# Optimization experiments

Measured on AMD Instinct MI355X. Metric: run time of the kernel, lower is better.

Reference implementation:

```python
import jax, jax.numpy as jnp
import numpy as np

B, N, DIM, HEADS = 8, 512, 512, 16
MAX_DIST, NG = 128, 32
RBF_STOP = 20.0
EPS = 1e-5


def _ln(x, g, b):
    m = jnp.mean(x, axis=-1, keepdims=True)
    v = jnp.mean((x - m) ** 2, axis=-1, keepdims=True)
    return (x - m) * jax.lax.rsqrt(v + EPS) * g + b


def setup_inputs() -> dict:
    key = jax.random.key(0)
    ks = jax.random.split(key, 12)
    d = DIM
    s = 0.02
    return {
        "x": jax.random.normal(ks[0], (B * N, d), jnp.float32),
        "dist_matrix": jax.random.randint(ks[1], (B, N, N), 0, MAX_DIST, jnp.int32),
        "dist_3d": jax.random.uniform(ks[2], (B, N, N), jnp.float32) * RBF_STOP,
        "norm1_g": jnp.ones((d,), jnp.float32),
        "norm1_b": jnp.zeros((d,), jnp.float32),
        "in_proj_w": jax.random.normal(ks[3], (3 * d, d), jnp.float32) * s,
        "in_proj_b": jnp.zeros((3 * d,), jnp.float32),
        "out_proj_w": jax.random.normal(ks[4], (d, d), jnp.float32) * s,
        "out_proj_b": jnp.zeros((d,), jnp.float32),
        "dist_emb": jax.random.normal(ks[5], (MAX_DIST, HEADS), jnp.float32) * s,
        "rbf_w": jax.random.normal(ks[6], (HEADS, NG), jnp.float32) * s,
        "rbf_b": jnp.zeros((HEADS,), jnp.float32),
        "norm2_g": jnp.ones((d,), jnp.float32),
        "norm2_b": jnp.zeros((d,), jnp.float32),
        "ffn_w1": jax.random.normal(ks[7], (4 * d, d), jnp.float32) * s,
        "ffn_b1": jnp.zeros((4 * d,), jnp.float32),
        "ffn_w2": jax.random.normal(ks[8], (d, 4 * d), jnp.float32) * s,
        "ffn_b2": jnp.zeros((d,), jnp.float32),
        "batch": jnp.repeat(jnp.arange(B, dtype=jnp.int32), N),
    }


def reference(x, dist_matrix, dist_3d, norm1_g, norm1_b, in_proj_w, in_proj_b,
              out_proj_w, out_proj_b, dist_emb, rbf_w, rbf_b, norm2_g, norm2_b,
              ffn_w1, ffn_b1, ffn_w2, ffn_b2, batch):
    b, n = dist_matrix.shape[0], dist_matrix.shape[1]
    d = x.shape[-1]
    dh = d // HEADS
    # equal-size graphs -> to_dense_batch is a reshape, mask all-true
    xd = x.reshape(b, n, d)

    # additive attention bias: shortest-path-distance embedding + RBF projection
    dc = jnp.clip(dist_matrix, 0, MAX_DIST - 1)
    bias_spd = dist_emb[dc]                                  # [b, n, n, H]
    offset = jnp.linspace(0.0, RBF_STOP, NG, dtype=jnp.float32)
    coeff = -0.5 / (RBF_STOP / (NG - 1)) ** 2
    rbf = jnp.exp(coeff * (dist_3d[..., None] - offset) ** 2)  # [b, n, n, NG]
    bias_3d = rbf @ rbf_w.T + rbf_b                          # [b, n, n, H]
    bias = jnp.transpose(bias_spd + bias_3d, (0, 3, 1, 2))   # [b, H, n, n]

    # multi-head attention (pre-norm residual, as in source)
    h = _ln(xd, norm1_g, norm1_b)
    qkv = h @ in_proj_w.T + in_proj_b
    q, k, v = jnp.split(qkv, 3, axis=-1)
    q = q.reshape(b, n, HEADS, dh).transpose(0, 2, 1, 3)
    k = k.reshape(b, n, HEADS, dh).transpose(0, 2, 1, 3)
    v = v.reshape(b, n, HEADS, dh).transpose(0, 2, 1, 3)
    scores = jnp.einsum('bhqd,bhkd->bhqk', q, k) / jnp.sqrt(jnp.float32(dh)) + bias
    attn = jax.nn.softmax(scores, axis=-1)
    ctx = jnp.einsum('bhqk,bhkd->bhqd', attn, v)
    ctx = ctx.transpose(0, 2, 1, 3).reshape(b, n, d)
    attn_out = ctx @ out_proj_w.T + out_proj_b
    h = h + attn_out

    # FFN (dropout inactive at eval)
    h2 = _ln(h, norm2_g, norm2_b)
    ff = jax.nn.gelu(h2 @ ffn_w1.T + ffn_b1, approximate=False) @ ffn_w2.T + ffn_b2
    h = h + ff
    return h.reshape(b * n, d)
```

## Files before the change

kernel.cpp:

```cpp
#include <hip/hip_runtime.h>
#include <hip/hip_bf16.h>
#include <math.h>

#define BB 8
#define NN 512
#define DD 512
#define NH 16
#define DH 32
#define TD 1536
#define NG 32
#define MAXD 128

typedef __attribute__((ext_vector_type(8))) short bf16x8;
typedef __attribute__((ext_vector_type(4))) float f32x4;

__device__ inline short f2bf(float x) {
    __hip_bfloat16 h = __float2bfloat16(x);
    return *reinterpret_cast<short*>(&h);
}

__device__ inline void gld_lds16(const void* g, void* l) {
    __builtin_amdgcn_global_load_lds(
        (const __attribute__((address_space(1))) unsigned int*)g,
        (__attribute__((address_space(3))) unsigned int*)l, 16, 0, 0);
}

__global__ __launch_bounds__(256) void cvt_weights(
    const float* __restrict__ s0, const float* __restrict__ s1,
    const float* __restrict__ s2, const float* __restrict__ s3,
    short* __restrict__ d0, short* __restrict__ d1,
    short* __restrict__ d2, short* __restrict__ d3,
    int n0, int n1, int n2, int n3) {
    const float* s; short* d; int n;
    switch (blockIdx.y) {
        case 0: s = s0; d = d0; n = n0; break;
        case 1: s = s1; d = d1; n = n1; break;
        case 2: s = s2; d = d2; n = n2; break;
        default: s = s3; d = d3; n = n3; break;
    }
    const int i = (blockIdx.x * 256 + threadIdx.x) * 4;
    if (i >= n) return;
    const float4 v = *(const float4*)(s + i);
    short4 o;
    o.x = f2bf(v.x); o.y = f2bf(v.y); o.z = f2bf(v.z); o.w = f2bf(v.w);
    *(short4*)(d + i) = o;
}

__global__ __launch_bounds__(256) void ln_kernel(const float* __restrict__ x,
                                                 const float* __restrict__ g,
                                                 const float* __restrict__ b,
                                                 short* __restrict__ out_bf,
                                                 float* __restrict__ out_f) {
    const int row = blockIdx.x;
    const int tid = threadIdx.x;
    const float* xr = x + (size_t)row * DD;
    float v0 = xr[tid], v1 = xr[tid + 256];
    __shared__ float s1[256], s2[256];
    s1[tid] = v0 + v1;
    s2[tid] = v0 * v0 + v1 * v1;
    __syncthreads();
    for (int off = 128; off > 0; off >>= 1) {
        if (tid < off) { s1[tid] += s1[tid + off]; s2[tid] += s2[tid + off]; }
        __syncthreads();
    }
    const float mean = s1[0] * (1.0f / DD);
    const float var  = s2[0] * (1.0f / DD) - mean * mean;
    const float rs   = rsqrtf(var + 1e-5f);
    const float o0 = (v0 - mean) * rs * g[tid] + b[tid];
    const float o1 = (v1 - mean) * rs * g[tid + 256] + b[tid + 256];
    out_bf[(size_t)row * DD + tid]       = f2bf(o0);
    out_bf[(size_t)row * DD + tid + 256] = f2bf(o1);
    if (out_f) {
        out_f[(size_t)row * DD + tid]       = o0;
        out_f[(size_t)row * DD + tid + 256] = o1;
    }
}

template <bool GELU, bool RES, bool OUTBF>
__global__ __launch_bounds__(256) void gemm_bf16(
    const short* __restrict__ A, const short* __restrict__ Bw,
    const float* __restrict__ bias, const float* __restrict__ res,
    void* __restrict__ Cout, int M, int Nout, int K) {
    const int bm = blockIdx.y * 128;
    const int bn = blockIdx.x * 128;
    const int tid  = threadIdx.x;
    const int wave = tid >> 6;
    const int lane = tid & 63;
    const int l16  = lane & 15;
    const int quad = lane >> 4;
    const int wr = (wave >> 1) * 64;
    const int wc = (wave & 1) * 64;

    __shared__ short As[128 * 32];
    __shared__ short Bs[128 * 32];

    f32x4 acc[4][4];
#pragma unroll
    for (int i = 0; i < 4; i++)
#pragma unroll
        for (int j = 0; j < 4; j++) acc[i][j] = (f32x4){0.f, 0.f, 0.f, 0.f};

    for (int k0 = 0; k0 < K; k0 += 32) {
        const short* Ab = A + (size_t)bm * K + k0;
        const short* Bb = Bw + (size_t)bn * K + k0;
#pragma unroll
        for (int j = 0; j < 2; j++) {
            const int idx = j * 256 + wave * 64 + lane;
            const int row = idx >> 2, c = idx & 3;
            short* dstA = (short*)As + (size_t)(j * 256 + wave * 64) * 8;
            short* dstB = (short*)Bs + (size_t)(j * 256 + wave * 64) * 8;
            gld_lds16(Ab + (size_t)row * K + c * 8, dstA);
            gld_lds16(Bb + (size_t)row * K + c * 8, dstB);
        }
        __syncthreads();
        bf16x8 af[4], bfr[4];
#pragma unroll
        for (int i = 0; i < 4; i++)
            af[i] = *(const bf16x8*)&As[(wr + i * 16 + l16) * 32 + quad * 8];
#pragma unroll
        for (int j = 0; j < 4; j++)
            bfr[j] = *(const bf16x8*)&Bs[(wc + j * 16 + l16) * 32 + quad * 8];
#pragma unroll
        for (int i = 0; i < 4; i++)
#pragma unroll
            for (int j = 0; j < 4; j++)
                acc[i][j] = __builtin_amdgcn_mfma_f32_16x16x32_bf16(af[i], bfr[j], acc[i][j], 0, 0, 0);
        __syncthreads();
    }
#pragma unroll
    for (int i = 0; i < 4; i++) {
#pragma unroll
        for (int r = 0; r < 4; r++) {
            const int row = bm + wr + i * 16 + quad * 4 + r;
#pragma unroll
            for (int j = 0; j < 4; j++) {
                const int col = bn + wc + j * 16 + l16;
                float v = acc[i][j][r] + bias[col];
                if (GELU) v = 0.5f * v * (1.0f + erff(v * 0.70710678118654752f));
                if (RES)  v += res[(size_t)row * Nout + col];
                if (OUTBF) ((short*)Cout)[(size_t)row * Nout + col] = f2bf(v);
                else       ((float*)Cout)[(size_t)row * Nout + col] = v;
            }
        }
    }
}

__global__ __launch_bounds__(512) void attn_mfma(
    const short* __restrict__ qkv,
    const int* __restrict__ dist,
    const float* __restrict__ dist3d,
    const float* __restrict__ demb,
    const float* __restrict__ rbfw,
    const float* __restrict__ rbfb,
    float* __restrict__ O_part,
    float* __restrict__ l_part)
{
    const int blk  = blockIdx.x;
    const int b    = blk & 7;
    const int half = (blk >> 3) & 1;
    const int q0   = (blk >> 4) * 16;
    const int tid  = threadIdx.x;
    const int wave = tid >> 6;
    const int lane = tid & 63;
    const int l16  = lane & 15;
    const int quad = lane >> 4;

    __shared__ short Kc[NH * 16 * 32];
    __shared__ short Vc[NH * 16 * 32];
    __shared__ float biasT[16 * 16 * 17];
    __shared__ short Pb[8 * 16 * 32];

    for (int i = tid; i < 8 * 16 * 32; i += 512) Pb[i] = 0;

    const float scale = 0.17677669529663687f;
    bf16x8 qf[2];
#pragma unroll
    for (int h = 0; h < 2; h++) {
        const int hh = wave * 2 + h;
        qf[h] = *(const bf16x8*)(qkv + (size_t)(b * NN + q0 + l16) * TD + hh * DH + quad * 8);
    }
    bf16x8 wf;
#pragma unroll
    for (int j = 0; j < 8; j++) wf[j] = f2bf(rbfw[l16 * NG + quad * 8 + j]);

    f32x4 O[2][2];
    float lsum[2][4];
#pragma unroll
    for (int h = 0; h < 2; h++) {
#pragma unroll
        for (int t = 0; t < 2; t++) O[h][t] = (f32x4){0.f, 0.f, 0.f, 0.f};
#pragma unroll
        for (int r = 0; r < 4; r++) lsum[h][r] = 0.f;
    }

    const float STEP  = 20.0f / 31.0f;
    const float COEFF = -0.5f / (STEP * STEP);

    for (int c = 0; c < 16; c++) {
        const int k0 = half * 256 + c * 16;
        __syncthreads();
#pragma unroll
        for (int l = 0; l < 4; l++) {
            const int idxb = l * 512 + wave * 64;
            const int idx  = idxb + lane;
            const int kk2  = idx & 1023;
            const int h = kk2 >> 6, k = (kk2 >> 2) & 15, c4 = kk2 & 3;
            const short* src = qkv + (size_t)(b * NN + k0 + k) * TD +
                               DD * (1 + (l >> 1)) + h * 32 + c4 * 8;
            short* dstb = (l < 2 ? (short*)Kc : (short*)Vc) + (size_t)(idxb & 1023) * 8;
            gld_lds16(src, dstb);
        }
#pragma unroll
        for (int g = 0; g < 2; g++) {
            const int qloc = wave * 2 + g;
            const size_t rowbase = ((size_t)(b * NN) + q0 + qloc) * NN + k0;
            const float d3 = dist3d[rowbase + l16];
            bf16x8 ef;
#pragma unroll
            for (int j = 0; j < 8; j++) {
                const float t = d3 - (float)(quad * 8 + j) * STEP;
                ef[j] = f2bf(__expf(COEFF * t * t));
            }
            f32x4 cc;
            const float rb = rbfb[l16];
#pragma unroll
            for (int r = 0; r < 4; r++) {
                int dc = dist[rowbase + quad * 4 + r];
                dc = min(max(dc, 0), MAXD - 1);
                cc[r] = demb[dc * NH + l16] + rb;
            }
            const f32x4 dres = __builtin_amdgcn_mfma_f32_16x16x32_bf16(ef, wf, cc, 0, 0, 0);
#pragma unroll
            for (int r = 0; r < 4; r++)
                biasT[(qloc * 16 + quad * 4 + r) * 17 + l16] = dres[r];
        }
        __syncthreads();
#pragma unroll
        for (int h = 0; h < 2; h++) {
            const int hh = wave * 2 + h;
            const bf16x8 kf = *(const bf16x8*)&Kc[hh * 512 + l16 * 32 + quad * 8];
            f32x4 s = __builtin_amdgcn_mfma_f32_16x16x32_bf16(
                qf[h], kf, (f32x4){0.f, 0.f, 0.f, 0.f}, 0, 0, 0);
            float pv[4];
#pragma unroll
            for (int r = 0; r < 4; r++) {
                float sv = s[r] * scale + biasT[((quad * 4 + r) * 16 + l16) * 17 + hh];
                sv = fminf(sv, 20.f);
                pv[r] = __expf(sv);
                lsum[h][r] += pv[r];
                Pb[wave * 512 + (quad * 4 + r) * 32 + l16] = f2bf(pv[r]);
            }
            const bf16x8 pf = *(const bf16x8*)&Pb[wave * 512 + l16 * 32 + quad * 8];
#pragma unroll
            for (int t = 0; t < 2; t++) {
                bf16x8 vf;
                if (quad < 2) {
#pragma unroll
                    for (int j = 0; j < 8; j++)
                        vf[j] = Vc[hh * 512 + (quad * 8 + j) * 32 + t * 16 + l16];
                } else {
#pragma unroll
                    for (int j = 0; j < 8; j++) vf[j] = 0;
                }
                O[h][t] = __builtin_amdgcn_mfma_f32_16x16x32_bf16(pf, vf, O[h][t], 0, 0, 0);
            }
        }
    }
    const size_t halfoff = (size_t)half * 4096;
#pragma unroll
    for (int h = 0; h < 2; h++) {
        const int hh = wave * 2 + h;
#pragma unroll
        for (int m = 1; m < 16; m <<= 1)
#pragma unroll
            for (int r = 0; r < 4; r++) lsum[h][r] += __shfl_xor(lsum[h][r], m);
#pragma unroll
        for (int r = 0; r < 4; r++) {
            const size_t row = (size_t)(b * NN + q0 + quad * 4 + r);
#pragma unroll
            for (int t = 0; t < 2; t++)
                O_part[(halfoff + row) * DD + hh * DH + t * 16 + l16] = O[h][t][r];
            if (l16 == 0) l_part[(halfoff + row) * NH + hh] = lsum[h][r];
        }
    }
}

__global__ __launch_bounds__(256) void attn_combine(
    const float* __restrict__ O_part, const float* __restrict__ l_part,
    short* __restrict__ ctx) {
    const int e = (blockIdx.x * 256 + threadIdx.x) * 4;
    const int row = e >> 9, d = e & 511, h = d >> 5;
    const float4 o0 = *(const float4*)(O_part + e);
    const float4 o1 = *(const float4*)(O_part + (size_t)4096 * 512 + e);
    const float l = l_part[row * NH + h] + l_part[4096 * NH + row * NH + h];
    const float rinv = 1.0f / l;
    short4 o;
    o.x = f2bf((o0.x + o1.x) * rinv);
    o.y = f2bf((o0.y + o1.y) * rinv);
    o.z = f2bf((o0.z + o1.z) * rinv);
    o.w = f2bf((o0.w + o1.w) * rinv);
    *(short4*)(ctx + e) = o;
}

extern "C" void kernel_launch(void* const* d_in, const int* in_sizes, int n_in,
                              void* d_out, int out_size, void* d_ws, size_t ws_size,
                              hipStream_t stream) {
    const float* x      = (const float*)d_in[0];
    const int*   dist   = (const int*)d_in[1];
    const float* dist3d = (const float*)d_in[2];
    const float* n1g    = (const float*)d_in[3];
    const float* n1b    = (const float*)d_in[4];
    const float* win    = (const float*)d_in[5];
    const float* bin    = (const float*)d_in[6];
    const float* wo     = (const float*)d_in[7];
    const float* bo     = (const float*)d_in[8];
    const float* demb   = (const float*)d_in[9];
    const float* rbfw   = (const float*)d_in[10];
    const float* rbfb   = (const float*)d_in[11];
    const float* n2g    = (const float*)d_in[12];
    const float* n2b    = (const float*)d_in[13];
    const float* w1     = (const float*)d_in[14];
    const float* b1     = (const float*)d_in[15];
    const float* w2     = (const float*)d_in[16];
    const float* b2     = (const float*)d_in[17];

    char* p = (char*)d_ws;
    short* h_bf   = (short*)p; p += (size_t)4096 * 512 * 2;
    float* h_f    = (float*)p; p += (size_t)4096 * 512 * 4;
    short* qkv_bf = (short*)p; p += (size_t)4096 * 1536 * 2;
    short* ctx_bf = (short*)p; p += (size_t)4096 * 512 * 2;
    float* hres   = (float*)p; p += (size_t)4096 * 512 * 4;
    short* h2_bf  = (short*)p; p += (size_t)4096 * 512 * 2;
    short* mid_bf = (short*)p; p += (size_t)4096 * 2048 * 2;
    short* win_bf = (short*)p; p += (size_t)1536 * 512 * 2;
    short* wo_bf  = (short*)p; p += (size_t)512 * 512 * 2;
    short* w1_bf  = (short*)p; p += (size_t)2048 * 512 * 2;
    short* w2_bf  = (short*)p; p += (size_t)512 * 2048 * 2;
    float* O_part = (float*)p; p += (size_t)2 * 4096 * 512 * 4;
    float* l_part = (float*)p; p += (size_t)2 * 4096 * 16 * 4;

    const int M = BB * NN;

    cvt_weights<<<dim3(1024, 4), 256, 0, stream>>>(
        win, wo, w1, w2, win_bf, wo_bf, w1_bf, w2_bf,
        1536 * 512, 512 * 512, 2048 * 512, 512 * 2048);
    ln_kernel<<<M, 256, 0, stream>>>(x, n1g, n1b, h_bf, h_f);
    gemm_bf16<false, false, true><<<dim3(12, 32), 256, 0, stream>>>(
        h_bf, win_bf, bin, nullptr, qkv_bf, M, TD, DD);
    attn_mfma<<<512, 512, 0, stream>>>(
        qkv_bf, dist, dist3d, demb, rbfw, rbfb, O_part, l_part);
    attn_combine<<<2048, 256, 0, stream>>>(O_part, l_part, ctx_bf);
    gemm_bf16<false, true, false><<<dim3(4, 32), 256, 0, stream>>>(
        ctx_bf, wo_bf, bo, h_f, hres, M, DD, DD);
    ln_kernel<<<M, 256, 0, stream>>>(hres, n2g, n2b, h2_bf, nullptr);
    gemm_bf16<true, false, true><<<dim3(16, 32), 256, 0, stream>>>(
        h2_bf, w1_bf, b1, nullptr, mid_bf, M, 2048, DD);
    gemm_bf16<false, true, false><<<dim3(4, 32), 256, 0, stream>>>(
        mid_bf, w2_bf, b2, hres, (float*)d_out, M, DD, 2048);
}
```

Baseline: 282.3 us.

## Write V transposed from QKV GEMM, bf16 bias tile, smaller M tiles for N=512 GEMMs

The QKV GEMM epilogue now writes V transposed per batch ([b][h*dh][n]) into a separate buffer, and Q/K into a 1024-wide buffer. The attention kernel can then load V fragments as vector LDS reads instead of eight strided scalar reads. The bias tile in LDS is stored as bf16 with padding, which cuts shared memory, and launch bounds request higher occupancy. The out-proj and FFN2 GEMMs use 64-row tiles so twice as many blocks run, at the cost of less B-operand reuse. Rounding the bias to bf16 slightly lowers precision.

After: 336.0 us. 19.0% more time.

```diff
diff --git a/kernel.cpp b/kernel.cpp
--- a/kernel.cpp
+++ b/kernel.cpp
@@ -7,7 +7,6 @@
 #define DD 512
 #define NH 16
 #define DH 32
-#define TD 1536
 #define NG 32
 #define MAXD 128
 
@@ -17,6 +16,11 @@
 __device__ inline short f2bf(float x) {
     __hip_bfloat16 h = __float2bfloat16(x);
     return *reinterpret_cast<short*>(&h);
+}
+__device__ inline float bf2f(short x) {
+    union { unsigned u; float f; } c;
+    c.u = ((unsigned)(unsigned short)x) << 16;
+    return c.f;
 }
 
 __device__ inline void gld_lds16(const void* g, void* l) {
@@ -76,27 +80,29 @@
     }
 }
 
-template <bool GELU, bool RES, bool OUTBF>
+template <int TM, bool GELU, bool RES, int OUT>
 __global__ __launch_bounds__(256) void gemm_bf16(
     const short* __restrict__ A, const short* __restrict__ Bw,
     const float* __restrict__ bias, const float* __restrict__ res,
-    void* __restrict__ Cout, int M, int Nout, int K) {
-    const int bm = blockIdx.y * 128;
+    void* __restrict__ Cout, short* __restrict__ vt,
+    int M, int Nout, int K) {
+    const int MI = TM / 32;
+    const int bm = blockIdx.y * TM;
     const int bn = blockIdx.x * 128;
     const int tid  = threadIdx.x;
     const int wave = tid >> 6;
     const int lane = tid & 63;
     const int l16  = lane & 15;
     const int quad = lane >> 4;
-    const int wr = (wave >> 1) * 64;
+    const int wr = (wave >> 1) * (TM / 2);
     const int wc = (wave & 1) * 64;
 
-    __shared__ short As[128 * 32];
+    __shared__ short As[TM * 32];
     __shared__ short Bs[128 * 32];
 
-    f32x4 acc[4][4];
-#pragma unroll
-    for (int i = 0; i < 4; i++)
+    f32x4 acc[MI][4];
+#pragma unroll
+    for (int i = 0; i < MI; i++)
 #pragma unroll
         for (int j = 0; j < 4; j++) acc[i][j] = (f32x4){0.f, 0.f, 0.f, 0.f};
 
@@ -104,49 +110,66 @@
         const short* Ab = A + (size_t)bm * K + k0;
         const short* Bb = Bw + (size_t)bn * K + k0;
 #pragma unroll
+        for (int j = 0; j < TM / 64; j++) {
+            const int idx = j * 256 + wave * 64 + lane;
+            gld_lds16(Ab + (size_t)(idx >> 2) * K + (idx & 3) * 8,
+                      (short*)As + (size_t)(j * 256 + wave * 64) * 8);
+        }
+#pragma unroll
         for (int j = 0; j < 2; j++) {
             const int idx = j * 256 + wave * 64 + lane;
-            const int row = idx >> 2, c = idx & 3;
-            short* dstA = (short*)As + (size_t)(j * 256 + wave * 64) * 8;
-            short* dstB = (short*)Bs + (size_t)(j * 256 + wave * 64) * 8;
-            gld_lds16(Ab + (size_t)row * K + c * 8, dstA);
-            gld_lds16(Bb + (size_t)row * K + c * 8, dstB);
-        }
-        __syncthreads();
-        bf16x8 af[4], bfr[4];
-#pragma unroll
-        for (int i = 0; i < 4; i++)
+            gld_lds16(Bb + (size_t)(idx >> 2) * K + (idx & 3) * 8,
+                      (short*)Bs + (size_t)(j * 256 + wave * 64) * 8);
+        }
+        __syncthreads();
+        bf16x8 af[MI], bfr[4];
+#pragma unroll
+        for (int i = 0; i < MI; i++)
             af[i] = *(const bf16x8*)&As[(wr + i * 16 + l16) * 32 + quad * 8];
 #pragma unroll
         for (int j = 0; j < 4; j++)
             bfr[j] = *(const bf16x8*)&Bs[(wc + j * 16 + l16) * 32 + quad * 8];
 #pragma unroll
-        for (int i = 0; i < 4; i++)
+        for (int i = 0; i < MI; i++)
 #pragma unroll
             for (int j = 0; j < 4; j++)
                 acc[i][j] = __builtin_amdgcn_mfma_f32_16x16x32_bf16(af[i], bfr[j], acc[i][j], 0, 0, 0);
         __syncthreads();
     }
 #pragma unroll
-    for (int i = 0; i < 4; i++) {
-#pragma unroll
-        for (int r = 0; r < 4; r++) {
-            const int row = bm + wr + i * 16 + quad * 4 + r;
-#pragma unroll
-            for (int j = 0; j < 4; j++) {
-                const int col = bn + wc + j * 16 + l16;
-                float v = acc[i][j][r] + bias[col];
-                if (GELU) v = 0.5f * v * (1.0f + erff(v * 0.70710678118654752f));
-                if (RES)  v += res[(size_t)row * Nout + col];
-                if (OUTBF) ((short*)Cout)[(size_t)row * Nout + col] = f2bf(v);
-                else       ((float*)Cout)[(size_t)row * Nout + col] = v;
-            }
-        }
-    }
-}
-
-__global__ __launch_bounds__(512) void attn_mfma(
-    const short* __restrict__ qkv,
+    for (int i = 0; i < MI; i++) {
+#pragma unroll
+        for (int j = 0; j < 4; j++) {
+            const int col = bn + wc + j * 16 + l16;
+            if (OUT == 2 && col >= 1024) {
+                const int n0 = bm + wr + i * 16 + quad * 4;
+                const int cv = col - 1024;
+                const float bv = bias[col];
+                short4 o;
+                o.x = f2bf(acc[i][j][0] + bv);
+                o.y = f2bf(acc[i][j][1] + bv);
+                o.z = f2bf(acc[i][j][2] + bv);
+                o.w = f2bf(acc[i][j][3] + bv);
+                *(short4*)&vt[((size_t)(n0 >> 9) * 512 + cv) * 512 + (n0 & 511)] = o;
+            } else {
+#pragma unroll
+                for (int r = 0; r < 4; r++) {
+                    const int row = bm + wr + i * 16 + quad * 4 + r;
+                    float v = acc[i][j][r] + bias[col];
+                    if (GELU) v = 0.5f * v * (1.0f + erff(v * 0.70710678118654752f));
+                    if (RES)  v += res[(size_t)row * Nout + col];
+                    if (OUT == 2)      ((short*)Cout)[(size_t)row * 1024 + col] = f2bf(v);
+                    else if (OUT == 1) ((short*)Cout)[(size_t)row * Nout + col] = f2bf(v);
+                    else               ((float*)Cout)[(size_t)row * Nout + col] = v;
+                }
+            }
+        }
+    }
+}
+
+__global__ __launch_bounds__(512, 6) void attn_mfma(
+    const short* __restrict__ qk,
+    const short* __restrict__ vt,
     const int* __restrict__ dist,
     const float* __restrict__ dist3d,
     const float* __restrict__ demb,
@@ -166,8 +189,8 @@
     const int quad = lane >> 4;
 
     __shared__ short Kc[NH * 16 * 32];
-    __shared__ short Vc[NH * 16 * 32];
-    __shared__ float biasT[16 * 16 * 17];
+    __shared__ short Vt[NH * 32 * 16];
+    __shared__ short biasB[16 * 16 * 24];
     __shared__ short Pb[8 * 16 * 32];
 
     for (int i = tid; i < 8 * 16 * 32; i += 512) Pb[i] = 0;
@@ -177,7 +200,7 @@
 #pragma unroll
     for (int h = 0; h < 2; h++) {
         const int hh = wave * 2 + h;
-        qf[h] = *(const bf16x8*)(qkv + (size_t)(b * NN + q0 + l16) * TD + hh * DH + quad * 8);
+        qf[h] = *(const bf16x8*)(qk + (size_t)(b * NN + q0 + l16) * 1024 + hh * DH + quad * 8);
     }
     bf16x8 wf;
 #pragma unroll
@@ -203,12 +226,16 @@
         for (int l = 0; l < 4; l++) {
             const int idxb = l * 512 + wave * 64;
             const int idx  = idxb + lane;
-            const int kk2  = idx & 1023;
-            const int h = kk2 >> 6, k = (kk2 >> 2) & 15, c4 = kk2 & 3;
-            const short* src = qkv + (size_t)(b * NN + k0 + k) * TD +
-                               DD * (1 + (l >> 1)) + h * 32 + c4 * 8;
-            short* dstb = (l < 2 ? (short*)Kc : (short*)Vc) + (size_t)(idxb & 1023) * 8;
-            gld_lds16(src, dstb);
+            if (l < 2) {
+                const int h = idx >> 6, k = (idx >> 2) & 15, c4 = idx & 3;
+                const short* src = qk + (size_t)(b * NN + k0 + k) * 1024 + 512 + h * DH + c4 * 8;
+                gld_lds16(src, (short*)Kc + (size_t)idxb * 8);
+            } else {
+                const int vi = idx - 1024;
+                const int hd = vi >> 1, c2 = vi & 1;
+                const short* src = vt + ((size_t)b * 512 + hd) * 512 + k0 + c2 * 8;
+                gld_lds16(src, (short*)Vt + (size_t)(idxb - 1024) * 8);
+            }
         }
 #pragma unroll
         for (int g = 0; g < 2; g++) {
@@ -232,19 +259,19 @@
             const f32x4 dres = __builtin_amdgcn_mfma_f32_16x16x32_bf16(ef, wf, cc, 0, 0, 0);
 #pragma unroll
             for (int r = 0; r < 4; r++)
-                biasT[(qloc * 16 + quad * 4 + r) * 17 + l16] = dres[r];
+                biasB[(qloc * 16 + quad * 4 + r) * 24 + l16] = f2bf(dres[r]);
         }
         __syncthreads();
 #pragma unroll
         for (int h = 0; h < 2; h++) {
             const int hh = wave * 2 + h;
-            const bf16x8 kf = *(const bf16x8*)&Kc[hh * 512 + l16 * 32 + quad * 8];
+            const bf16x8 kf = *(const bf16x8*)&Kc[(hh * 16 + l16) * 32 + quad * 8];
             f32x4 s = __builtin_amdgcn_mfma_f32_16x16x32_bf16(
                 qf[h], kf, (f32x4){0.f, 0.f, 0.f, 0.f}, 0, 0, 0);
             float pv[4];
 #pragma unroll
             for (int r = 0; r < 4; r++) {
-                float sv = s[r] * scale + biasT[((quad * 4 + r) * 16 + l16) * 17 + hh];
+                float sv = s[r] * scale + bf2f(biasB[((quad * 4 + r) * 16 + l16) * 24 + hh]);
                 sv = fminf(sv, 20.f);
                 pv[r] = __expf(sv);
                 lsum[h][r] += pv[r];
@@ -255,9 +282,7 @@
             for (int t = 0; t < 2; t++) {
                 bf16x8 vf;
                 if (quad < 2) {
-#pragma unroll
-                    for (int j = 0; j < 8; j++)
-                        vf[j] = Vc[hh * 512 + (quad * 8 + j) * 32 + t * 16 + l16];
+                    vf = *(const bf16x8*)&Vt[(hh * 32 + t * 16 + l16) * 16 + quad * 8];
                 } else {
 #pragma unroll
                     for (int j = 0; j < 8; j++) vf[j] = 0;
@@ -327,7 +352,8 @@
     char* p = (char*)d_ws;
     short* h_bf   = (short*)p; p += (size_t)4096 * 512 * 2;
     float* h_f    = (float*)p; p += (size_t)4096 * 512 * 4;
-    short* qkv_bf = (short*)p; p += (size_t)4096 * 1536 * 2;
+    short* qk_bf  = (short*)p; p += (size_t)4096 * 1024 * 2;
+    short* vt_bf  = (short*)p; p += (size_t)4096 * 512 * 2;
     short* ctx_bf = (short*)p; p += (size_t)4096 * 512 * 2;
     float* hres   = (float*)p; p += (size_t)4096 * 512 * 4;
     short* h2_bf  = (short*)p; p += (size_t)4096 * 512 * 2;
@@ -345,16 +371,16 @@
         win, wo, w1, w2, win_bf, wo_bf, w1_bf, w2_bf,
         1536 * 512, 512 * 512, 2048 * 512, 512 * 2048);
     ln_kernel<<<M, 256, 0, stream>>>(x, n1g, n1b, h_bf, h_f);
-    gemm_bf16<false, false, true><<<dim3(12, 32), 256, 0, stream>>>(
-        h_bf, win_bf, bin, nullptr, qkv_bf, M, TD, DD);
+    gemm_bf16<128, false, false, 2><<<dim3(12, 32), 256, 0, stream>>>(
+        h_bf, win_bf, bin, nullptr, qk_bf, vt_bf, M, 1536, DD);
     attn_mfma<<<512, 512, 0, stream>>>(
-        qkv_bf, dist, dist3d, demb, rbfw, rbfb, O_part, l_part);
+        qk_bf, vt_bf, dist, dist3d, demb, rbfw, rbfb, O_part, l_part);
     attn_combine<<<2048, 256, 0, stream>>>(O_part, l_part, ctx_bf);
-    gemm_bf16<false, true, false><<<dim3(4, 32), 256, 0, stream>>>(
-        ctx_bf, wo_bf, bo, h_f, hres, M, DD, DD);
+    gemm_bf16<64, false, true, 0><<<dim3(4, 64), 256, 0, stream>>>(
+        ctx_bf, wo_bf, bo, h_f, hres, nullptr, M, DD, DD);
     ln_kernel<<<M, 256, 0, stream>>>(hres, n2g, n2b, h2_bf, nullptr);
-    gemm_bf16<true, false, true><<<dim3(16, 32), 256, 0, stream>>>(
-        h2_bf, w1_bf, b1, nullptr, mid_bf, M, 2048, DD);
-    gemm_bf16<false, true, false><<<dim3(4, 32), 256, 0, stream>>>(
-        mid_bf, w2_bf, b2, hres, (float*)d_out, M, DD, 2048);
-}
+    gemm_bf16<128, true, false, 1><<<dim3(16, 32), 256, 0, stream>>>(
+        h2_bf, w1_bf, b1, nullptr, mid_bf, nullptr, M, 2048, DD);
+    gemm_bf16<64, false, true, 0><<<dim3(4, 64), 256, 0, stream>>>(
+        mid_bf, w2_bf, b2, hres, (float*)d_out, nullptr, M, DD, 2048);
+}
```

## Split attention keys four ways, use 64-row GEMM tiles, store bias as bf16

Applied to the files above, without the earlier changes.

The attention kernel now splits the key range into four parts instead of two, doubling the grid to 1024 blocks, and the combine kernel sums four partial outputs. The two narrow-output GEMMs (out-proj and FFN down) use 64-row tiles, doubling their block counts to raise occupancy across CUs. The attention bias tile in LDS is stored as bf16 instead of padded fp32 to shrink shared memory, and the mid buffer aliases the enlarged O_part workspace. The cost is more partial-sum traffic, extra combine reads, and some loss of bias precision.

New measurement: 277.3 us. About the same (-1.8%).

```diff
diff --git a/kernel.cpp b/kernel.cpp
--- a/kernel.cpp
+++ b/kernel.cpp
@@ -17,6 +17,11 @@
 __device__ inline short f2bf(float x) {
     __hip_bfloat16 h = __float2bfloat16(x);
     return *reinterpret_cast<short*>(&h);
+}
+__device__ inline float bf2f(short x) {
+    union { unsigned u; float f; } c;
+    c.u = ((unsigned)(unsigned short)x) << 16;
+    return c.f;
 }
 
 __device__ inline void gld_lds16(const void* g, void* l) {
@@ -76,27 +81,28 @@
     }
 }
 
-template <bool GELU, bool RES, bool OUTBF>
+template <int TM, bool GELU, bool RES, int OUT>
 __global__ __launch_bounds__(256) void gemm_bf16(
     const short* __restrict__ A, const short* __restrict__ Bw,
     const float* __restrict__ bias, const float* __restrict__ res,
     void* __restrict__ Cout, int M, int Nout, int K) {
-    const int bm = blockIdx.y * 128;
+    const int MI = TM / 32;
+    const int bm = blockIdx.y * TM;
     const int bn = blockIdx.x * 128;
     const int tid  = threadIdx.x;
     const int wave = tid >> 6;
     const int lane = tid & 63;
     const int l16  = lane & 15;
     const int quad = lane >> 4;
-    const int wr = (wave >> 1) * 64;
+    const int wr = (wave >> 1) * (TM / 2);
     const int wc = (wave & 1) * 64;
 
-    __shared__ short As[128 * 32];
+    __shared__ short As[TM * 32];
     __shared__ short Bs[128 * 32];
 
-    f32x4 acc[4][4];
-#pragma unroll
-    for (int i = 0; i < 4; i++)
+    f32x4 acc[MI][4];
+#pragma unroll
+    for (int i = 0; i < MI; i++)
 #pragma unroll
         for (int j = 0; j < 4; j++) acc[i][j] = (f32x4){0.f, 0.f, 0.f, 0.f};
 
@@ -104,31 +110,34 @@
         const short* Ab = A + (size_t)bm * K + k0;
         const short* Bb = Bw + (size_t)bn * K + k0;
 #pragma unroll
+        for (int j = 0; j < TM / 64; j++) {
+            const int idx = j * 256 + wave * 64 + lane;
+            gld_lds16(Ab + (size_t)(idx >> 2) * K + (idx & 3) * 8,
+                      (short*)As + (size_t)(j * 256 + wave * 64) * 8);
+        }
+#pragma unroll
         for (int j = 0; j < 2; j++) {
             const int idx = j * 256 + wave * 64 + lane;
-            const int row = idx >> 2, c = idx & 3;
-            short* dstA = (short*)As + (size_t)(j * 256 + wave * 64) * 8;
-            short* dstB = (short*)Bs + (size_t)(j * 256 + wave * 64) * 8;
-            gld_lds16(Ab + (size_t)row * K + c * 8, dstA);
-            gld_lds16(Bb + (size_t)row * K + c * 8, dstB);
-        }
-        __syncthreads();
-        bf16x8 af[4], bfr[4];
-#pragma unroll
-        for (int i = 0; i < 4; i++)
+            gld_lds16(Bb + (size_t)(idx >> 2) * K + (idx & 3) * 8,
+                      (short*)Bs + (size_t)(j * 256 + wave * 64) * 8);
+        }
+        __syncthreads();
+        bf16x8 af[MI], bfr[4];
+#pragma unroll
+        for (int i = 0; i < MI; i++)
             af[i] = *(const bf16x8*)&As[(wr + i * 16 + l16) * 32 + quad * 8];
 #pragma unroll
         for (int j = 0; j < 4; j++)
             bfr[j] = *(const bf16x8*)&Bs[(wc + j * 16 + l16) * 32 + quad * 8];
 #pragma unroll
-        for (int i = 0; i < 4; i++)
+        for (int i = 0; i < MI; i++)
 #pragma unroll
             for (int j = 0; j < 4; j++)
                 acc[i][j] = __builtin_amdgcn_mfma_f32_16x16x32_bf16(af[i], bfr[j], acc[i][j], 0, 0, 0);
         __syncthreads();
     }
 #pragma unroll
-    for (int i = 0; i < 4; i++) {
+    for (int i = 0; i < MI; i++) {
 #pragma unroll
         for (int r = 0; r < 4; r++) {
             const int row = bm + wr + i * 16 + quad * 4 + r;
@@ -138,8 +147,8 @@
                 float v = acc[i][j][r] + bias[col];
                 if (GELU) v = 0.5f * v * (1.0f + erff(v * 0.70710678118654752f));
                 if (RES)  v += res[(size_t)row * Nout + col];
-                if (OUTBF) ((short*)Cout)[(size_t)row * Nout + col] = f2bf(v);
-                else       ((float*)Cout)[(size_t)row * Nout + col] = v;
+                if (OUT == 1) ((short*)Cout)[(size_t)row * Nout + col] = f2bf(v);
+                else          ((float*)Cout)[(size_t)row * Nout + col] = v;
             }
         }
     }
@@ -157,8 +166,8 @@
 {
     const int blk  = blockIdx.x;
     const int b    = blk & 7;
-    const int half = (blk >> 3) & 1;
-    const int q0   = (blk >> 4) * 16;
+    const int part = (blk >> 3) & 3;
+    const int q0   = (blk >> 5) * 16;
     const int tid  = threadIdx.x;
     const int wave = tid >> 6;
     const int lane = tid & 63;
@@ -167,7 +176,7 @@
 
     __shared__ short Kc[NH * 16 * 32];
     __shared__ short Vc[NH * 16 * 32];
-    __shared__ float biasT[16 * 16 * 17];
+    __shared__ short biasB[16 * 16 * 24];
     __shared__ short Pb[8 * 16 * 32];
 
     for (int i = tid; i < 8 * 16 * 32; i += 512) Pb[i] = 0;
@@ -196,8 +205,8 @@
     const float STEP  = 20.0f / 31.0f;
     const float COEFF = -0.5f / (STEP * STEP);
 
-    for (int c = 0; c < 16; c++) {
-        const int k0 = half * 256 + c * 16;
+    for (int c = 0; c < 8; c++) {
+        const int k0 = part * 128 + c * 16;
         __syncthreads();
 #pragma unroll
         for (int l = 0; l < 4; l++) {
@@ -232,7 +241,7 @@
             const f32x4 dres = __builtin_amdgcn_mfma_f32_16x16x32_bf16(ef, wf, cc, 0, 0, 0);
 #pragma unroll
             for (int r = 0; r < 4; r++)
-                biasT[(qloc * 16 + quad * 4 + r) * 17 + l16] = dres[r];
+                biasB[(qloc * 16 + quad * 4 + r) * 24 + l16] = f2bf(dres[r]);
         }
         __syncthreads();
 #pragma unroll
@@ -244,7 +253,7 @@
             float pv[4];
 #pragma unroll
             for (int r = 0; r < 4; r++) {
-                float sv = s[r] * scale + biasT[((quad * 4 + r) * 16 + l16) * 17 + hh];
+                float sv = s[r] * scale + bf2f(biasB[((quad * 4 + r) * 16 + l16) * 24 + hh]);
                 sv = fminf(sv, 20.f);
                 pv[r] = __expf(sv);
                 lsum[h][r] += pv[r];
@@ -266,7 +275,7 @@
             }
         }
     }
-    const size_t halfoff = (size_t)half * 4096;
+    const size_t poff = (size_t)part * 4096;
 #pragma unroll
     for (int h = 0; h < 2; h++) {
         const int hh = wave * 2 + h;
@@ -279,8 +288,8 @@
             const size_t row = (size_t)(b * NN + q0 + quad * 4 + r);
 #pragma unroll
             for (int t = 0; t < 2; t++)
-                O_part[(halfoff + row) * DD + hh * DH + t * 16 + l16] = O[h][t][r];
-            if (l16 == 0) l_part[(halfoff + row) * NH + hh] = lsum[h][r];
+                O_part[(poff + row) * DD + hh * DH + t * 16 + l16] = O[h][t][r];
+            if (l16 == 0) l_part[(poff + row) * NH + hh] = lsum[h][r];
         }
     }
 }
@@ -290,15 +299,20 @@
     short* __restrict__ ctx) {
     const int e = (blockIdx.x * 256 + threadIdx.x) * 4;
     const int row = e >> 9, d = e & 511, h = d >> 5;
+    const size_t PO = (size_t)4096 * 512;
     const float4 o0 = *(const float4*)(O_part + e);
-    const float4 o1 = *(const float4*)(O_part + (size_t)4096 * 512 + e);
-    const float l = l_part[row * NH + h] + l_part[4096 * NH + row * NH + h];
+    const float4 o1 = *(const float4*)(O_part + PO + e);
+    const float4 o2 = *(const float4*)(O_part + 2 * PO + e);
+    const float4 o3 = *(const float4*)(O_part + 3 * PO + e);
+    const int li = row * NH + h;
+    const float l = l_part[li] + l_part[4096 * NH + li] +
+                    l_part[2 * 4096 * NH + li] + l_part[3 * 4096 * NH + li];
     const float rinv = 1.0f / l;
     short4 o;
-    o.x = f2bf((o0.x + o1.x) * rinv);
-    o.y = f2bf((o0.y + o1.y) * rinv);
-    o.z = f2bf((o0.z + o1.z) * rinv);
-    o.w = f2bf((o0.w + o1.w) * rinv);
+    o.x = f2bf((o0.x + o1.x + o2.x + o3.x) * rinv);
+    o.y = f2bf((o0.y + o1.y + o2.y + o3.y) * rinv);
+    o.z = f2bf((o0.z + o1.z + o2.z + o3.z) * rinv);
+    o.w = f2bf((o0.w + o1.w + o2.w + o3.w) * rinv);
     *(short4*)(ctx + e) = o;
 }
 
@@ -331,13 +345,14 @@
     short* ctx_bf = (short*)p; p += (size_t)4096 * 512 * 2;
     float* hres   = (float*)p; p += (size_t)4096 * 512 * 4;
     short* h2_bf  = (short*)p; p += (size_t)4096 * 512 * 2;
-    short* mid_bf = (short*)p; p += (size_t)4096 * 2048 * 2;
     short* win_bf = (short*)p; p += (size_t)1536 * 512 * 2;
     short* wo_bf  = (short*)p; p += (size_t)512 * 512 * 2;
     short* w1_bf  = (short*)p; p += (size_t)2048 * 512 * 2;
     short* w2_bf  = (short*)p; p += (size_t)512 * 2048 * 2;
-    float* O_part = (float*)p; p += (size_t)2 * 4096 * 512 * 4;
-    float* l_part = (float*)p; p += (size_t)2 * 4096 * 16 * 4;
+    float* O_part = (float*)p;
+    short* mid_bf = (short*)p;
+    p += (size_t)4 * 4096 * 512 * 4;
+    float* l_part = (float*)p; p += (size_t)4 * 4096 * 16 * 4;
 
     const int M = BB * NN;
 
@@ -345,16 +360,16 @@
         win, wo, w1, w2, win_bf, wo_bf, w1_bf, w2_bf,
         1536 * 512, 512 * 512, 2048 * 512, 512 * 2048);
     ln_kernel<<<M, 256, 0, stream>>>(x, n1g, n1b, h_bf, h_f);
-    gemm_bf16<false, false, true><<<dim3(12, 32), 256, 0, stream>>>(
+    gemm_bf16<128, false, false, 1><<<dim3(12, 32), 256, 0, stream>>>(
         h_bf, win_bf, bin, nullptr, qkv_bf, M, TD, DD);
-    attn_mfma<<<512, 512, 0, stream>>>(
+    attn_mfma<<<1024, 512, 0, stream>>>(
         qkv_bf, dist, dist3d, demb, rbfw, rbfb, O_part, l_part);
     attn_combine<<<2048, 256, 0, stream>>>(O_part, l_part, ctx_bf);
-    gemm_bf16<false, true, false><<<dim3(4, 32), 256, 0, stream>>>(
+    gemm_bf16<64, false, true, 0><<<dim3(4, 64), 256, 0, stream>>>(
         ctx_bf, wo_bf, bo, h_f, hres, M, DD, DD);
     ln_kernel<<<M, 256, 0, stream>>>(hres, n2g, n2b, h2_bf, nullptr);
-    gemm_bf16<true, false, true><<<dim3(16, 32), 256, 0, stream>>>(
+    gemm_bf16<128, true, false, 1><<<dim3(16, 32), 256, 0, stream>>>(
         h2_bf, w1_bf, b1, nullptr, mid_bf, M, 2048, DD);
-    gemm_bf16<false, true, false><<<dim3(4, 32), 256, 0, stream>>>(
+    gemm_bf16<64, false, true, 0><<<dim3(4, 64), 256, 0, stream>>>(
         mid_bf, w2_bf, b2, hres, (float*)d_out, M, DD, 2048);
 }
```
